# Kernel optimization log

Hardware: AMD Instinct MI355X
Metric: run time of the kernel (lower is better)

Reference implementation:

```python
import jax, jax.numpy as jnp
import numpy as np
from itertools import product

N_MFS_PER_UNIVERSE = [5, 5, 5]  # 3 universes x 5 membership functions -> F=15, R=125
B, S = 16, 2048


def _make_rules(n_mfs):
    # Faithful port of Rules.generate_rules: cartesian product over per-universe MF index
    # ranges, one-hot encoded into a (n_rules, total_mfs) binary matrix.
    offsets = np.concatenate([[0], np.cumsum(n_mfs)])
    ranges = [range(int(offsets[i]), int(offsets[i + 1])) for i in range(len(n_mfs))]
    combos = list(product(*ranges))
    rules = np.zeros((len(combos), int(offsets[-1])), dtype=np.float32)
    for i, combo in enumerate(combos):
        rules[i, list(combo)] = 1.0
    return jnp.asarray(rules)


def setup_inputs() -> dict:
    key = jax.random.key(0)
    F = sum(N_MFS_PER_UNIVERSE)
    x = jax.random.uniform(key, (B, S, F), dtype=jnp.float32)  # membership degrees in [0,1)
    active_rules = _make_rules(N_MFS_PER_UNIVERSE)  # (125, 15) one-hot-per-universe mask
    return {"x": x, "active_rules": active_rules, "epoch": 0}


def reference(x, active_rules, epoch):
    # relate_fuzzy_numbers: (B,S,1,F) * (R,F) -> (B,S,R,F), vectorized over the
    # original double Python loop over batch and universe dims.
    rpu = x[:, :, None, :] * active_rules[None, None, :, :]
    # larsen intersection: fuzzy product over selected membership functions.
    # Masked-out (zero) entries act as multiplicative identity.
    fired = jnp.prod(jnp.where(rpu == 0.0, 1.0, rpu), axis=-1)  # (B,S,R)
    # original: intersection keeps last dim then forward takes [:, :, :, 0]
    return fired
```

## Files before the change

kernel.cpp:

```cpp
#include <hip/hip_runtime.h>


__global__ __launch_bounds__(256) void rules_fired_kernel(
    const float* __restrict__ x, float* __restrict__ out, int total4) {
    int idx = blockIdx.x * blockDim.x + threadIdx.x;
    if (idx >= total4) return;
    int base = idx * 4;

    float4 v;
    float* vp = &v.x;
#pragma unroll
    for (int t = 0; t < 4; ++t) {
        int o = base + t;
        int bs = o / 125;
        int r = o - bs * 125;
        int i = r / 25;
        int rem = r - i * 25;
        int j = rem / 5;
        int k = rem - j * 5;
        const float* xp = x + bs * 15;
        float a = xp[i];
        float b = xp[5 + j];
        float c = xp[10 + k];
        a = (a == 0.0f) ? 1.0f : a;
        b = (b == 0.0f) ? 1.0f : b;
        c = (c == 0.0f) ? 1.0f : c;
        vp[t] = (a * b) * c;
    }
    *reinterpret_cast<float4*>(out + base) = v;
}

extern "C" void kernel_launch(void* const* d_in, const int* in_sizes, int n_in,
                              void* d_out, int out_size, void* d_ws, size_t ws_size,
                              hipStream_t stream) {
    const float* x = (const float*)d_in[0];
    float* out = (float*)d_out;

    int total4 = out_size / 4;
    int block = 256;
    int grid = (total4 + block - 1) / block;
    rules_fired_kernel<<<grid, block, 0, stream>>>(x, out, total4);
}
```

Measured before the change: 67.63 us.

## Stage input rows and pairwise products in shared memory per block

Each block now handles 32 rows. It loads their 15 inputs into LDS with float4 loads, applying the zero-to-one substitution once per input. It then precomputes the 25 first-two-universe products per row, and each output needs only one multiply from LDS. This removes the repeated scattered global loads and redundant divisions of the old one-thread-per-4-outputs scheme. The cost is two block barriers, and the code assumes the row count is a multiple of 32 with no tail handling.

After: 65.28 us. 1.04x faster.

```diff
diff --git a/kernel.cpp b/kernel.cpp
--- a/kernel.cpp
+++ b/kernel.cpp
@@ -1,33 +1,53 @@
 #include <hip/hip_runtime.h>
 
 
+#define ROWS_PER_BLOCK 32
+
 __global__ __launch_bounds__(256) void rules_fired_kernel(
-    const float* __restrict__ x, float* __restrict__ out, int total4) {
-    int idx = blockIdx.x * blockDim.x + threadIdx.x;
-    if (idx >= total4) return;
-    int base = idx * 4;
+    const float* __restrict__ x, float* __restrict__ out) {
+    __shared__ float xs[ROWS_PER_BLOCK * 15];
+    __shared__ float pij[ROWS_PER_BLOCK * 25];
 
-    float4 v;
-    float* vp = &v.x;
+    const int tid = threadIdx.x;
+    const int row0 = blockIdx.x * ROWS_PER_BLOCK;
+
+    if (tid < 120) {
+        float4 v = reinterpret_cast<const float4*>(x + row0 * 15)[tid];
+        v.x = (v.x == 0.0f) ? 1.0f : v.x;
+        v.y = (v.y == 0.0f) ? 1.0f : v.y;
+        v.z = (v.z == 0.0f) ? 1.0f : v.z;
+        v.w = (v.w == 0.0f) ? 1.0f : v.w;
+        reinterpret_cast<float4*>(xs)[tid] = v;
+    }
+    __syncthreads();
+
+    for (int t = tid; t < ROWS_PER_BLOCK * 25; t += 256) {
+        int row = t / 25;
+        int u = t - row * 25;
+        int i = u / 5;
+        int j = u - i * 5;
+        pij[t] = xs[row * 15 + i] * xs[row * 15 + 5 + j];
+    }
+    __syncthreads();
+
+    float4* outv = reinterpret_cast<float4*>(out + row0 * 125);
+    for (int s = tid; s < 1000; s += 256) {
+        int o = s * 4;
+        int row = o / 125;
+        int r = o - row * 125;
+        float4 v;
+        float* vp = &v.x;
 #pragma unroll
-    for (int t = 0; t < 4; ++t) {
-        int o = base + t;
-        int bs = o / 125;
-        int r = o - bs * 125;
-        int i = r / 25;
-        int rem = r - i * 25;
-        int j = rem / 5;
-        int k = rem - j * 5;
-        const float* xp = x + bs * 15;
-        float a = xp[i];
-        float b = xp[5 + j];
-        float c = xp[10 + k];
-        a = (a == 0.0f) ? 1.0f : a;
-        b = (b == 0.0f) ? 1.0f : b;
-        c = (c == 0.0f) ? 1.0f : c;
-        vp[t] = (a * b) * c;
+        for (int t2 = 0; t2 < 4; ++t2) {
+            int rr = r + t2;
+            int rowa = row;
+            if (rr >= 125) { rowa += 1; rr -= 125; }
+            int u = rr / 5;
+            int k = rr - u * 5;
+            vp[t2] = pij[rowa * 25 + u] * xs[rowa * 15 + 10 + k];
+        }
+        outv[s] = v;
     }
-    *reinterpret_cast<float4*>(out + base) = v;
 }
 
 extern "C" void kernel_launch(void* const* d_in, const int* in_sizes, int n_in,
@@ -36,8 +56,7 @@
     const float* x = (const float*)d_in[0];
     float* out = (float*)d_out;
 
-    int total4 = out_size / 4;
-    int block = 256;
-    int grid = (total4 + block - 1) / block;
-    rules_fired_kernel<<<grid, block, 0, stream>>>(x, out, total4);
+    int n_rows = out_size / 125;
+    int grid = n_rows / ROWS_PER_BLOCK;
+    rules_fired_kernel<<<grid, 256, 0, stream>>>(x, out);
 }
```
